# Performance work log

Measured on AMD Instinct MI355X. Metric: run time of the kernel, lower is better.

## Reference

```python
import jax, jax.numpy as jnp
import numpy as np

N = 50000      # nodes
IN = 128       # in_channels
H = 2          # heads
C = 64         # hidden_channels (per head)
E = 800000     # edges (before self-loops)
OUT = 40       # out_channels
BN_EPS = 1e-5
NEG_SLOPE = 0.2  # PyG GATConv default


def _bn(x, g, b):
    # BatchNorm1d forward with batch statistics (training-mode math, biased var)
    mu = jnp.mean(x, axis=0)
    v = jnp.var(x, axis=0)
    return (x - mu) * jax.lax.rsqrt(v + BN_EPS) * g + b


def _gat_conv(x, src, dst, W, a_src, a_dst, bias, concat):
    n = x.shape[0]
    h = (x @ W).reshape(n, H, C)                      # [N,H,C] per-head projection
    al_s = jnp.einsum('nhc,hc->nh', h, a_src)         # [N,H]
    al_d = jnp.einsum('nhc,hc->nh', h, a_dst)
    e = jax.nn.leaky_relu(al_s[src] + al_d[dst], NEG_SLOPE)  # [E,H]
    # segment softmax over edges sharing the same destination
    m = jax.ops.segment_max(e, dst, num_segments=n)
    ex = jnp.exp(e - m[dst])
    s = jax.ops.segment_sum(ex, dst, num_segments=n)
    alpha = ex / s[dst]                               # [E,H]
    out = jax.ops.segment_sum(h[src] * alpha[..., None], dst, num_segments=n)  # [N,H,C]
    out = out.reshape(n, H * C) if concat else out.mean(axis=1)
    return out + bias


def setup_inputs() -> dict:
    key = jax.random.key(0)
    ks = jax.random.split(key, 16)
    g = lambda k, shp, scale=1.0: jax.random.normal(k, shp, dtype=jnp.float32) * scale
    x = g(ks[0], (N, IN))
    edge_index = jax.random.randint(ks[1], (2, E), 0, N, dtype=jnp.int32)
    s = 1.0 / np.sqrt(IN)
    s2 = 1.0 / np.sqrt(H * C)
    return {
        'x': x,
        'edge_index': edge_index,
        'bn0_g': jnp.ones((IN,), jnp.float32), 'bn0_b': jnp.zeros((IN,), jnp.float32),
        'W1': g(ks[2], (IN, H * C), s), 'a1_src': g(ks[3], (H, C), s), 'a1_dst': g(ks[4], (H, C), s),
        'b1': jnp.zeros((H * C,), jnp.float32),
        'bn1_g': jnp.ones((H * C,), jnp.float32), 'bn1_b': jnp.zeros((H * C,), jnp.float32),
        'W2': g(ks[5], (H * C, H * C), s2), 'a2_src': g(ks[6], (H, C), s2), 'a2_dst': g(ks[7], (H, C), s2),
        'b2': jnp.zeros((C,), jnp.float32),
        'bn2_g': jnp.ones((C,), jnp.float32), 'bn2_b': jnp.zeros((C,), jnp.float32),
        'Wf': g(ks[8], (C, OUT), 1.0 / np.sqrt(C)), 'bf': jnp.zeros((OUT,), jnp.float32),
    }


def reference(x, edge_index, bn0_g, bn0_b, W1, a1_src, a1_dst, b1, bn1_g, bn1_b,
              W2, a2_src, a2_dst, b2, bn2_g, bn2_b, Wf, bf):
    n = x.shape[0]
    loop = jnp.arange(n, dtype=edge_index.dtype)
    src = jnp.concatenate([edge_index[0], loop])  # add self-loops (PyG default)
    dst = jnp.concatenate([edge_index[1], loop])
    h = _bn(x, bn0_g, bn0_b)
    # layer 1: concat heads
    h = _gat_conv(h, src, dst, W1, a1_src, a1_dst, b1, concat=True)
    h = jax.nn.elu(_bn(h, bn1_g, bn1_b))
    # (dropout is identity in eval mode)
    # layer 2: average heads
    h = _gat_conv(h, src, dst, W2, a2_src, a2_dst, b2, concat=False)
    h = jax.nn.elu(_bn(h, bn2_g, bn2_b))
    return h @ Wf + bf
```

## Files before the change

kernel.cpp:

```cpp
#include <hip/hip_runtime.h>
#include <hip/hip_fp16.h>


#define NEG_SLOPE 0.2f
#define BN_EPS 1e-5f
#define SH 15
#define NRANGE 16

typedef short bf16x8 __attribute__((ext_vector_type(8)));
typedef float f32x4 __attribute__((ext_vector_type(4)));

static __device__ __forceinline__ unsigned short f2bf(float f) {
    union { float f; unsigned u; } v; v.f = f;
    unsigned r = v.u + 0x7FFF + ((v.u >> 16) & 1);
    return (unsigned short)(r >> 16);
}
static __device__ __forceinline__ float2 bf2x2(unsigned v) {
    union { unsigned u; float f; } a, b;
    a.u = v << 16; b.u = v & 0xffff0000u;
    return make_float2(a.f, b.f);
}
static __device__ __forceinline__ float halfsel(unsigned p, int head) {
    __half2 h = *(__half2*)&p;
    return head ? __high2float(h) : __low2float(h);
}

template <int C>
static __device__ __forceinline__ void d_bnstat(const float* __restrict__ x, int M,
                                                int rowsPerBlock, float* __restrict__ sums,
                                                int b, float* red) {
    constexpr int TPR = C / 4;
    constexpr int RS  = 256 / TPR;
    const int t = threadIdx.x;
    const int cg = t % TPR, rg = t / TPR, w = t >> 6, lane = t & 63;
    int r0 = b * rowsPerBlock + rg;
    int r1 = min(M, b * rowsPerBlock + rowsPerBlock);
    float4 s = make_float4(0, 0, 0, 0), q = make_float4(0, 0, 0, 0);
    #pragma unroll 4
    for (int r = r0; r < r1; r += RS) {
        float4 v = *(const float4*)&x[(size_t)r * C + cg * 4];
        s.x += v.x; s.y += v.y; s.z += v.z; s.w += v.w;
        q.x += v.x * v.x; q.y += v.y * v.y; q.z += v.z * v.z; q.w += v.w * v.w;
    }
    #pragma unroll
    for (int off = TPR; off < 64; off <<= 1) {
        s.x += __shfl_xor(s.x, off); s.y += __shfl_xor(s.y, off);
        s.z += __shfl_xor(s.z, off); s.w += __shfl_xor(s.w, off);
        q.x += __shfl_xor(q.x, off); q.y += __shfl_xor(q.y, off);
        q.z += __shfl_xor(q.z, off); q.w += __shfl_xor(q.w, off);
    }
    if (lane < TPR) {
        *(float4*)&red[w * 2 * C + cg * 4] = s;
        *(float4*)&red[w * 2 * C + C + cg * 4] = q;
    }
    __syncthreads();
    for (int idx = t; idx < 2 * C; idx += 256) {
        float tot = red[idx] + red[2 * C + idx] + red[4 * C + idx] + red[6 * C + idx];
        atomicAdd(&sums[idx], tot);
    }
}

template <int C>
__global__ __launch_bounds__(256) void k_bnstat2(const float* __restrict__ x, int M,
                                                 int rowsPerBlock, float* __restrict__ sums) {
    __shared__ __align__(16) float red[4 * 2 * C];
    d_bnstat<C>(x, M, rowsPerBlock, sums, blockIdx.x, red);
}

__global__ __launch_bounds__(256) void k_prep(
    const int* __restrict__ ei, int E, int S, int NR,
    const float* __restrict__ x, int M, int bgrid,
    const float* __restrict__ W1, const float* __restrict__ W2,
    unsigned short* __restrict__ cnt, unsigned short* __restrict__ rank,
    float* __restrict__ sums,
    unsigned short* __restrict__ wt1, unsigned short* __restrict__ wt2) {
    __shared__ __align__(16) unsigned smem[3200];
    int b = blockIdx.x;
    int CG = NRANGE * S;
    if (b < CG) {
        unsigned* lcnt = smem;
        const int t = threadIdx.x;
        const int r = b & (NRANGE - 1), s = b >> 4;
        const unsigned lo = (unsigned)(r * NR);
        const int NRW = NR >> 1;
        for (int j = t; j < NRW; j += 256) lcnt[j] = 0;
        __syncthreads();
        int i1 = min(E, (s + 1) << SH);
        #pragma unroll 4
        for (int i = (s << SH) + t; i < i1; i += 256) {
            unsigned d = (unsigned)ei[E + i];
            unsigned rel = d - lo;
            if (rel < (unsigned)NR) {
                unsigned sh = (rel & 1) << 4;
                unsigned old = atomicAdd(&lcnt[rel >> 1], 1u << sh);
                rank[i] = (unsigned short)((old >> sh) & 0xffffu);
            }
        }
        __syncthreads();
        for (int j = t; j < NRW; j += 256) {
            int node = (int)lo + 2 * j;
            if (node < M)
                *(unsigned*)&cnt[(size_t)s * M + node] = lcnt[j];
        }
    } else if (b < CG + bgrid) {
        d_bnstat<128>(x, M, 256, sums, b - CG, (float*)smem);
    } else {
        int idx = (b - CG - bgrid) * 256 + threadIdx.x;
        if (idx < 128 * 128) {
            int n = idx >> 7, k = idx & 127;
            wt1[idx] = f2bf(W1[k * 128 + n]);
            wt2[idx] = f2bf(W2[k * 128 + n]);
        }
    }
}

__global__ __launch_bounds__(256) void k_scan(unsigned short* __restrict__ cnt,
                                              int Nn, int S,
                                              int* __restrict__ gcur,
                                              int* __restrict__ rowptr,
                                              unsigned short* __restrict__ degs) {
    __shared__ int wsum[4];
    __shared__ int s_base;
    int t = threadIdx.x, lane = t & 63, w = t >> 6;
    int i = blockIdx.x * 256 + t;
    int v = 0;
    if (i < Nn) {
        int run = 0;
        for (int s = 0; s < S; s++) {
            int cv = (int)cnt[(size_t)s * Nn + i];
            cnt[(size_t)s * Nn + i] = (unsigned short)run;
            run += cv;
        }
        v = run + 1;
    }
    int x = v;
    #pragma unroll
    for (int off = 1; off < 64; off <<= 1) {
        int y = __shfl_up(x, off);
        if (lane >= off) x += y;
    }
    if (lane == 63) wsum[w] = x;
    __syncthreads();
    if (t < 4) {
        int val = wsum[t];
        int xs = val;
        #pragma unroll
        for (int off = 1; off < 4; off <<= 1) {
            int y = __shfl_up(xs, off);
            if (t >= off) xs += y;
        }
        if (t == 3) s_base = atomicAdd(gcur, xs);
        wsum[t] = xs - val;
    }
    __syncthreads();
    if (i < Nn) {
        rowptr[i] = s_base + wsum[w] + (x - v);
        degs[i] = (unsigned short)v;
    }
}

static __device__ __forceinline__ void d_fill(int b, const int* __restrict__ ei,
                                              const unsigned short* __restrict__ rank,
                                              const unsigned short* __restrict__ pofs,
                                              const int* __restrict__ rowptr, int E, int Nn,
                                              unsigned short* __restrict__ ssrc) {
    int i = b * 256 + threadIdx.x;
    if (i < E) {
        int s = ei[i], d = ei[E + i];
        int p = i >> SH;
        int rk = (int)pofs[(size_t)p * Nn + d] + (int)rank[i];
        ssrc[rowptr[d] + 1 + rk] = (unsigned short)s;
    } else if (i < E + Nn) {
        int d = i - E;
        ssrc[rowptr[d]] = (unsigned short)d;
    }
}

static __device__ __forceinline__ void d_mfma(
    int blk, const float* __restrict__ A, const unsigned short* __restrict__ wt,
    const float* __restrict__ sums, const float* __restrict__ bng, const float* __restrict__ bnb,
    int elu, const float* __restrict__ asrc, const float* __restrict__ adst, int M,
    unsigned short* __restrict__ hb, float* __restrict__ als, float* __restrict__ ald) {
    __shared__ unsigned short As[64 * 136];
    __shared__ __align__(16) float stl[256];
    const int t = threadIdx.x;
    const int w = t >> 6, lane = t & 63;
    const int c = lane & 15, q = lane >> 4;
    const int row0 = blk * 64;

    if (t < 128) {
        float mu = sums[t] / (float)M;
        float var = sums[128 + t] / (float)M - mu * mu;
        float s = bng[t] * rsqrtf(var + BN_EPS);
        stl[t] = s;
        stl[128 + t] = bnb[t] - mu * s;
    }
    __syncthreads();

    const int gr = row0 + w * 16 + c;
    const bool rok = gr < M;

    float4 av[4][2];
    #pragma unroll
    for (int ks = 0; ks < 4; ks++) {
        const int cc = (ks * 4 + q) * 8;
        #pragma unroll
        for (int h = 0; h < 2; h++)
            av[ks][h] = rok ? *(const float4*)&A[(size_t)gr * 128 + cc + h * 4]
                            : make_float4(0.f, 0.f, 0.f, 0.f);
    }

    bf16x8 af[4];
    #pragma unroll
    for (int ks = 0; ks < 4; ks++) {
        const int cc = (ks * 4 + q) * 8;
        union { bf16x8 v; unsigned u[4]; } pk;
        #pragma unroll
        for (int h = 0; h < 2; h++) {
            float4 v = av[ks][h];
            if (rok) {
                float4 sc = *(const float4*)&stl[cc + h * 4];
                float4 sh = *(const float4*)&stl[128 + cc + h * 4];
                v.x = v.x * sc.x + sh.x; v.y = v.y * sc.y + sh.y;
                v.z = v.z * sc.z + sh.z; v.w = v.w * sc.w + sh.w;
                if (elu) {
                    v.x = v.x > 0.f ? v.x : expm1f(v.x);
                    v.y = v.y > 0.f ? v.y : expm1f(v.y);
                    v.z = v.z > 0.f ? v.z : expm1f(v.z);
                    v.w = v.w > 0.f ? v.w : expm1f(v.w);
                }
            }
            pk.u[h * 2]     = ((unsigned)f2bf(v.y) << 16) | f2bf(v.x);
            pk.u[h * 2 + 1] = ((unsigned)f2bf(v.w) << 16) | f2bf(v.z);
        }
        af[ks] = pk.v;
    }

    f32x4 acc[8] = {};
    #pragma unroll
    for (int half = 0; half < 2; half++) {
        bf16x8 br[8][2];
        #pragma unroll
        for (int tl = 0; tl < 8; tl++) {
            #pragma unroll
            for (int kk = 0; kk < 2; kk++)
                br[tl][kk] = *(const bf16x8*)&wt[(size_t)(tl * 16 + c) * 128 + ((half * 2 + kk) * 4 + q) * 8];
        }
        #pragma unroll
        for (int kk = 0; kk < 2; kk++) {
            #pragma unroll
            for (int tl = 0; tl < 8; tl++)
                acc[tl] = __builtin_amdgcn_mfma_f32_16x16x32_bf16(af[half * 2 + kk], br[tl][kk], acc[tl], 0, 0, 0);
        }
    }

    float as_[8], ad_[8];
    #pragma unroll
    for (int tl = 0; tl < 8; tl++) { as_[tl] = asrc[tl * 16 + c]; ad_[tl] = adst[tl * 16 + c]; }
    #pragma unroll
    for (int reg = 0; reg < 4; reg++) {
        float s0 = 0.f, s1 = 0.f, d0 = 0.f, d1 = 0.f;
        #pragma unroll
        for (int tl = 0; tl < 4; tl++) { s0 += acc[tl][reg] * as_[tl]; d0 += acc[tl][reg] * ad_[tl]; }
        #pragma unroll
        for (int tl = 4; tl < 8; tl++) { s1 += acc[tl][reg] * as_[tl]; d1 += acc[tl][reg] * ad_[tl]; }
        #pragma unroll
        for (int off = 1; off < 16; off <<= 1) {
            s0 += __shfl_xor(s0, off); s1 += __shfl_xor(s1, off);
            d0 += __shfl_xor(d0, off); d1 += __shfl_xor(d1, off);
        }
        int grow = row0 + w * 16 + q * 4 + reg;
        if (c == 0 && grow < M) {
            *(float2*)&als[(size_t)grow * 2] = make_float2(s0, s1);
            *(float2*)&ald[(size_t)grow * 2] = make_float2(d0, d1);
        }
    }

    #pragma unroll
    for (int reg = 0; reg < 4; reg++) {
        #pragma unroll
        for (int tl = 0; tl < 8; tl++)
            As[(w * 16 + q * 4 + reg) * 136 + tl * 16 + c] = f2bf(acc[tl][reg]);
    }
    #pragma unroll
    for (int j = 0; j < 4; j++) {
        int f = j * 64 + lane;
        int r = f >> 4, ch = f & 15;
        int grow = row0 + w * 16 + r;
        if (grow < M) {
            uint4 v = *(uint4*)&As[(w * 16 + r) * 136 + ch * 8];
            *(uint4*)&hb[(size_t)grow * 128 + ch * 8] = v;
        }
    }
}

__global__ __launch_bounds__(256) void k_mfma(
    const float* __restrict__ A, const unsigned short* __restrict__ wt,
    const float* __restrict__ sums, const float* __restrict__ bng, const float* __restrict__ bnb,
    int elu, const float* __restrict__ asrc, const float* __restrict__ adst, int M,
    unsigned short* __restrict__ hb, float* __restrict__ als, float* __restrict__ ald) {
    d_mfma(blockIdx.x, A, wt, sums, bng, bnb, elu, asrc, adst, M, hb, als, ald);
}

__global__ __launch_bounds__(256) void k_fill_mfma(
    const float* __restrict__ A, const unsigned short* __restrict__ wt,
    const float* __restrict__ sums, const float* __restrict__ bng, const float* __restrict__ bnb,
    const float* __restrict__ asrc, const float* __restrict__ adst, int M, int ggrid,
    unsigned short* __restrict__ hb, float* __restrict__ als, float* __restrict__ ald,
    const int* __restrict__ ei, const unsigned short* __restrict__ rank,
    const unsigned short* __restrict__ pofs,
    const int* __restrict__ rowptr, int E, int Nn, unsigned short* __restrict__ ssrc) {
    if (blockIdx.x < ggrid)
        d_mfma(blockIdx.x, A, wt, sums, bng, bnb, 0, asrc, adst, M, hb, als, ald);
    else
        d_fill(blockIdx.x - ggrid, ei, rank, pofs, rowptr, E, Nn, ssrc);
}

static __device__ __forceinline__ void acc8(float* acc, uint4 v, float a) {
    float2 p;
    p = bf2x2(v.x); acc[0] += a * p.x; acc[1] += a * p.y;
    p = bf2x2(v.y); acc[2] += a * p.x; acc[3] += a * p.y;
    p = bf2x2(v.z); acc[4] += a * p.x; acc[5] += a * p.y;
    p = bf2x2(v.w); acc[6] += a * p.x; acc[7] += a * p.y;
}

template <int MEAN>
static __device__ __forceinline__ void attnagg(
    const int* __restrict__ rowptr, const unsigned short* __restrict__ degs,
    const unsigned short* __restrict__ ssrc,
    const float* __restrict__ als, const float* __restrict__ ald,
    float* __restrict__ alpha, const unsigned short* __restrict__ hb,
    const float* __restrict__ bias, int Nn, float* __restrict__ out) {
    int gw = (blockIdx.x * blockDim.x + threadIdx.x) >> 6;
    if (gw >= Nn) return;
    int lane = threadIdx.x & 63;
    int sub = lane >> 4, c = lane & 15, head = c >> 3;
    int beg = rowptr[gw];
    int deg = (int)degs[gw];
    int end = beg + deg;
    float2 dv = *(const float2*)&ald[(size_t)gw * 2];
    float acc[8] = {};

    if (deg <= 64) {
        bool on = lane < deg;
        int eidx = beg + (on ? lane : 0);
        int sreg = (int)ssrc[eidx];
        float2 av = *(const float2*)&als[(size_t)sreg * 2];
        float v0 = av.x + dv.x; v0 = v0 > 0.f ? v0 : NEG_SLOPE * v0;
        float v1 = av.y + dv.y; v1 = v1 > 0.f ? v1 : NEG_SLOPE * v1;
        float p0 = on ? __expf(v0) : 0.f;
        float p1 = on ? __expf(v1) : 0.f;
        float t0 = p0, t1 = p1;
        #pragma unroll
        for (int off = 32; off; off >>= 1) {
            t0 += __shfl_xor(t0, off);
            t1 += __shfl_xor(t1, off);
        }
        __half2 hpk = __floats2half2_rn(p0 / t0, p1 / t1);
        unsigned pk = *(unsigned*)&hpk;

        int nit = (deg + 3) >> 2;
        int it = 0;
        for (; it + 4 <= nit; it += 4) {
            int s_[4]; float a_[4];
            #pragma unroll
            for (int u = 0; u < 4; u++) {
                int jj = (it + u) * 4 + sub;
                int ls = jj & 63;
                s_[u] = __shfl(sreg, ls);
                unsigned pw = (unsigned)__shfl(pk, ls);
                a_[u] = (jj < deg) ? halfsel(pw, head) : 0.f;
            }
            #pragma unroll
            for (int u = 0; u < 4; u++) {
                uint4 v = *(const uint4*)&hb[(size_t)s_[u] * 128 + c * 8];
                acc8(acc, v, a_[u]);
            }
        }
        for (; it < nit; it += 2) {
            const bool two = (it + 1) < nit;
            int s_[2]; float a_[2];
            #pragma unroll
            for (int u = 0; u < 2; u++) {
                if (u == 0 || two) {
                    int jj = (it + u) * 4 + sub;
                    int ls = jj & 63;
                    s_[u] = __shfl(sreg, ls);
                    unsigned pw = (unsigned)__shfl(pk, ls);
                    a_[u] = (jj < deg) ? halfsel(pw, head) : 0.f;
                }
            }
            #pragma unroll
            for (int u = 0; u < 2; u++) {
                if (u == 0 || two) {
                    uint4 v = *(const uint4*)&hb[(size_t)s_[u] * 128 + c * 8];
                    acc8(acc, v, a_[u]);
                }
            }
        }
    } else {
        float d0 = dv.x, d1 = dv.y;
        float m0 = -1e30f, m1 = -1e30f;
        for (int e = beg + lane; e < end; e += 64) {
            int s = (int)ssrc[e];
            float v0 = als[s * 2] + d0;     v0 = v0 > 0.f ? v0 : NEG_SLOPE * v0;
            float v1 = als[s * 2 + 1] + d1; v1 = v1 > 0.f ? v1 : NEG_SLOPE * v1;
            m0 = fmaxf(m0, v0); m1 = fmaxf(m1, v1);
        }
        #pragma unroll
        for (int off = 32; off; off >>= 1) {
            m0 = fmaxf(m0, __shfl_xor(m0, off));
            m1 = fmaxf(m1, __shfl_xor(m1, off));
        }
        float t0 = 0.f, t1 = 0.f;
        for (int e = beg + lane; e < end; e += 64) {
            int s = (int)ssrc[e];
            float v0 = als[s * 2] + d0;     v0 = v0 > 0.f ? v0 : NEG_SLOPE * v0;
            float v1 = als[s * 2 + 1] + d1; v1 = v1 > 0.f ? v1 : NEG_SLOPE * v1;
            float p0 = __expf(v0 - m0), p1 = __expf(v1 - m1);
            alpha[e * 2] = p0; alpha[e * 2 + 1] = p1;
            t0 += p0; t1 += p1;
        }
        #pragma unroll
        for (int off = 32; off; off >>= 1) {
            t0 += __shfl_xor(t0, off);
            t1 += __shfl_xor(t1, off);
        }
        float i0 = 1.f / t0, i1 = 1.f / t1;
        for (int e = beg + sub; e < end; e += 4) {
            int s = (int)ssrc[e];
            float a = (head ? alpha[(size_t)e * 2 + 1] * i1 : alpha[(size_t)e * 2] * i0);
            uint4 v = *(const uint4*)&hb[(size_t)s * 128 + c * 8];
            acc8(acc, v, a);
        }
    }

    #pragma unroll
    for (int j2 = 0; j2 < 8; j2++) {
        acc[j2] += __shfl_xor(acc[j2], 16);
        acc[j2] += __shfl_xor(acc[j2], 32);
        if (MEAN) acc[j2] += __shfl_xor(acc[j2], 8);
    }
    if (MEAN) {
        if (sub == 0 && c < 8) {
            float4 b0 = *(const float4*)&bias[c * 8];
            float4 b1 = *(const float4*)&bias[c * 8 + 4];
            float4 o0 = make_float4(0.5f * acc[0] + b0.x, 0.5f * acc[1] + b0.y, 0.5f * acc[2] + b0.z, 0.5f * acc[3] + b0.w);
            float4 o1 = make_float4(0.5f * acc[4] + b1.x, 0.5f * acc[5] + b1.y, 0.5f * acc[6] + b1.z, 0.5f * acc[7] + b1.w);
            *(float4*)&out[(size_t)gw * 64 + c * 8] = o0;
            *(float4*)&out[(size_t)gw * 64 + c * 8 + 4] = o1;
        }
    } else {
        if (sub == 0) {
            float4 b0 = *(const float4*)&bias[c * 8];
            float4 b1 = *(const float4*)&bias[c * 8 + 4];
            float4 o0 = make_float4(acc[0] + b0.x, acc[1] + b0.y, acc[2] + b0.z, acc[3] + b0.w);
            float4 o1 = make_float4(acc[4] + b1.x, acc[5] + b1.y, acc[6] + b1.z, acc[7] + b1.w);
            *(float4*)&out[(size_t)gw * 128 + c * 8] = o0;
            *(float4*)&out[(size_t)gw * 128 + c * 8 + 4] = o1;
        }
    }
}

__global__ __launch_bounds__(256) void k_attnagg1(const int* __restrict__ rowptr, const unsigned short* __restrict__ degs,
                                                  const unsigned short* __restrict__ ssrc,
                                                  const float* __restrict__ als, const float* __restrict__ ald,
                                                  float* __restrict__ alpha, const unsigned short* __restrict__ hb,
                                                  const float* __restrict__ bias, int Nn, float* __restrict__ out) {
    attnagg<0>(rowptr, degs, ssrc, als, ald, alpha, hb, bias, Nn, out);
}

__global__ __launch_bounds__(256) void k_attnagg2(const int* __restrict__ rowptr, const unsigned short* __restrict__ degs,
                                                  const unsigned short* __restrict__ ssrc,
                                                  const float* __restrict__ als, const float* __restrict__ ald,
                                                  float* __restrict__ alpha, const unsigned short* __restrict__ hb,
                                                  const float* __restrict__ bias, int Nn, float* __restrict__ out) {
    attnagg<1>(rowptr, degs, ssrc, als, ald, alpha, hb, bias, Nn, out);
}

__global__ __launch_bounds__(128) void k_gemmf(const float* __restrict__ A, const float* __restrict__ Wf,
                                               const float* __restrict__ bf,
                                               const float* __restrict__ sums, const float* __restrict__ bng,
                                               const float* __restrict__ bnb,
                                               int M, float* __restrict__ out) {
    __shared__ float As[128 * 65];
    __shared__ float Bs[64 * 40];
    __shared__ float stl[128];
    int t = threadIdx.x;
    int row0 = blockIdx.x * 128;
    if (t < 64) {
        float mu = sums[t] / (float)M;
        float var = sums[64 + t] / (float)M - mu * mu;
        float s = bng[t] * rsqrtf(var + BN_EPS);
        stl[t] = s;
        stl[64 + t] = bnb[t] - mu * s;
    }
    __syncthreads();
    for (int i = t; i < 64 * 40; i += 128) Bs[i] = Wf[i];
    for (int i = t; i < 128 * 64; i += 128) {
        int r = i >> 6, k = i & 63;
        int gr = row0 + r;
        float v = 0.f;
        if (gr < M) {
            v = A[(size_t)gr * 64 + k] * stl[k] + stl[64 + k];
            v = v > 0.f ? v : expm1f(v);
        }
        As[r * 65 + k] = v;
    }
    __syncthreads();
    int cg = t & 3, rg = t >> 2;
    float acc[4][10] = {};
    for (int k = 0; k < 64; k++) {
        float b[10];
        #pragma unroll
        for (int j = 0; j < 10; j++) b[j] = Bs[k * 40 + cg * 10 + j];
        #pragma unroll
        for (int r = 0; r < 4; r++) {
            float a = As[(rg * 4 + r) * 65 + k];
            #pragma unroll
            for (int j = 0; j < 10; j++) acc[r][j] += a * b[j];
        }
    }
    for (int r = 0; r < 4; r++) {
        int gr = row0 + rg * 4 + r;
        if (gr < M) {
            #pragma unroll
            for (int j = 0; j < 10; j++) out[(size_t)gr * 40 + cg * 10 + j] = acc[r][j] + bf[cg * 10 + j];
        }
    }
}

extern "C" void kernel_launch(void* const* d_in, const int* in_sizes, int n_in,
                              void* d_out, int out_size, void* d_ws, size_t ws_size,
                              hipStream_t stream) {
    const float* x     = (const float*)d_in[0];
    const int*   ei    = (const int*)d_in[1];
    const float* bn0_g = (const float*)d_in[2];
    const float* bn0_b = (const float*)d_in[3];
    const float* W1    = (const float*)d_in[4];
    const float* a1s   = (const float*)d_in[5];
    const float* a1d   = (const float*)d_in[6];
    const float* b1    = (const float*)d_in[7];
    const float* bn1_g = (const float*)d_in[8];
    const float* bn1_b = (const float*)d_in[9];
    const float* W2    = (const float*)d_in[10];
    const float* a2s   = (const float*)d_in[11];
    const float* a2d   = (const float*)d_in[12];
    const float* b2    = (const float*)d_in[13];
    const float* bn2_g = (const float*)d_in[14];
    const float* bn2_b = (const float*)d_in[15];
    const float* Wf    = (const float*)d_in[16];
    const float* bf    = (const float*)d_in[17];
    float* out = (float*)d_out;

    const int N  = in_sizes[0] / 128;
    const int E  = in_sizes[1] / 2;
    const int ET = E + N;
    const int S  = (E + (1 << SH) - 1) >> SH;
    const int NR = (((N + NRANGE - 1) / NRANGE) + 1) & ~1;

    char* ws = (char*)d_ws;
    size_t off = 0;
    auto alloc = [&](size_t bytes) -> char* {
        char* p = ws + off;
        off = (off + bytes + 255) & ~(size_t)255;
        return p;
    };
    float* sums   = (float*)alloc(644 * 4);
    int*   gcur   = (int*)(sums + 640);
    const size_t zlen = off;
    unsigned short* cnt = (unsigned short*)alloc((size_t)S * N * 2);
    int*   rowptr = (int*)alloc((size_t)N * 4);
    unsigned short* degs = (unsigned short*)alloc((size_t)N * 2);
    unsigned short* ssrc = (unsigned short*)alloc((size_t)ET * 2);
    unsigned short* rank = (unsigned short*)alloc((size_t)E * 2);
    float* abuf   = (float*)alloc((size_t)N * 128 * 4);
    unsigned short* hb  = (unsigned short*)alloc((size_t)N * 128 * 2);
    unsigned short* wt1 = (unsigned short*)alloc((size_t)128 * 128 * 2);
    unsigned short* wt2 = (unsigned short*)alloc((size_t)128 * 128 * 2);
    float* alpha  = (float*)alloc((size_t)ET * 2 * 4);
    float* als    = (float*)alloc((size_t)N * 2 * 4);
    float* ald    = (float*)alloc((size_t)N * 2 * 4);

    const int tb = 256;
    const int CG = NRANGE * S;
    const int bgrid = (N + 255) / 256;
    const int fgrid = (ET + tb - 1) / tb;
    const int wgrid = ((size_t)N * 64 + tb - 1) / tb;
    const int ggrid = (N + 63) / 64;

    hipMemsetAsync(ws, 0, zlen, stream);

    k_prep<<<CG + bgrid + 64, tb, 0, stream>>>(ei, E, S, NR, x, N, bgrid, W1, W2,
                                               cnt, rank, sums, wt1, wt2);
    k_scan<<<bgrid, tb, 0, stream>>>(cnt, N, S, gcur, rowptr, degs);

    k_fill_mfma<<<ggrid + fgrid, tb, 0, stream>>>(x, wt1, sums, bn0_g, bn0_b,
                                                  a1s, a1d, N, ggrid, hb, als, ald,
                                                  ei, rank, cnt, rowptr, E, N, ssrc);
    k_attnagg1<<<wgrid, tb, 0, stream>>>(rowptr, degs, ssrc, als, ald, alpha, hb, b1, N, abuf);

    k_bnstat2<128><<<bgrid, 256, 0, stream>>>(abuf, N, 256, sums + 256);

    k_mfma<<<ggrid, tb, 0, stream>>>(abuf, wt2, sums + 256, bn1_g, bn1_b, 1, a2s, a2d, N, hb, als, ald);
    k_attnagg2<<<wgrid, tb, 0, stream>>>(rowptr, degs, ssrc, als, ald, alpha, hb, b2, N, abuf);

    k_bnstat2<64><<<bgrid, 256, 0, stream>>>(abuf, N, 256, sums + 512);

    k_gemmf<<<(N + 127) / 128, 128, 0, stream>>>(abuf, Wf, bf, sums + 512, bn2_g, bn2_b, N, out);
}
```

Measured before the change: 349.4 us.

## Replace partitioned LDS counting sort with global atomic per-node counters

Edge-to-destination counting moves from a blocked scheme (edge chunks by node ranges, LDS 16-bit packed counters, per-chunk offsets scanned in k_scan) to one global int atomicAdd per edge that returns the rank directly. This removes the 16x re-reads of the destination array, the per-chunk count matrix and its serial per-node scan, and simplifies the fill step. In exchange it relies on global atomics contending on about 50k counters, and the order within each row becomes nondeterministic.

Result: faster. 332.6 us (-4.8%).

```diff
diff --git a/kernel.cpp b/kernel.cpp
--- a/kernel.cpp
+++ b/kernel.cpp
@@ -4,8 +4,6 @@
 
 #define NEG_SLOPE 0.2f
 #define BN_EPS 1e-5f
-#define SH 15
-#define NRANGE 16
 
 typedef short bf16x8 __attribute__((ext_vector_type(8)));
 typedef float f32x4 __attribute__((ext_vector_type(4)));
@@ -68,44 +66,24 @@
 }
 
 __global__ __launch_bounds__(256) void k_prep(
-    const int* __restrict__ ei, int E, int S, int NR,
+    const int* __restrict__ ei, int E, int rgrid,
     const float* __restrict__ x, int M, int bgrid,
     const float* __restrict__ W1, const float* __restrict__ W2,
-    unsigned short* __restrict__ cnt, unsigned short* __restrict__ rank,
+    int* __restrict__ cnt, unsigned short* __restrict__ rank,
     float* __restrict__ sums,
     unsigned short* __restrict__ wt1, unsigned short* __restrict__ wt2) {
-    __shared__ __align__(16) unsigned smem[3200];
+    __shared__ __align__(16) float red[4 * 2 * 128];
     int b = blockIdx.x;
-    int CG = NRANGE * S;
-    if (b < CG) {
-        unsigned* lcnt = smem;
-        const int t = threadIdx.x;
-        const int r = b & (NRANGE - 1), s = b >> 4;
-        const unsigned lo = (unsigned)(r * NR);
-        const int NRW = NR >> 1;
-        for (int j = t; j < NRW; j += 256) lcnt[j] = 0;
-        __syncthreads();
-        int i1 = min(E, (s + 1) << SH);
-        #pragma unroll 4
-        for (int i = (s << SH) + t; i < i1; i += 256) {
-            unsigned d = (unsigned)ei[E + i];
-            unsigned rel = d - lo;
-            if (rel < (unsigned)NR) {
-                unsigned sh = (rel & 1) << 4;
-                unsigned old = atomicAdd(&lcnt[rel >> 1], 1u << sh);
-                rank[i] = (unsigned short)((old >> sh) & 0xffffu);
-            }
-        }
-        __syncthreads();
-        for (int j = t; j < NRW; j += 256) {
-            int node = (int)lo + 2 * j;
-            if (node < M)
-                *(unsigned*)&cnt[(size_t)s * M + node] = lcnt[j];
-        }
-    } else if (b < CG + bgrid) {
-        d_bnstat<128>(x, M, 256, sums, b - CG, (float*)smem);
+    if (b < rgrid) {
+        int i = b * 256 + threadIdx.x;
+        if (i < E) {
+            int d = ei[E + i];
+            rank[i] = (unsigned short)atomicAdd(&cnt[d], 1);
+        }
+    } else if (b < rgrid + bgrid) {
+        d_bnstat<128>(x, M, 256, sums, b - rgrid, red);
     } else {
-        int idx = (b - CG - bgrid) * 256 + threadIdx.x;
+        int idx = (b - rgrid - bgrid) * 256 + threadIdx.x;
         if (idx < 128 * 128) {
             int n = idx >> 7, k = idx & 127;
             wt1[idx] = f2bf(W1[k * 128 + n]);
@@ -114,8 +92,7 @@
     }
 }
 
-__global__ __launch_bounds__(256) void k_scan(unsigned short* __restrict__ cnt,
-                                              int Nn, int S,
+__global__ __launch_bounds__(256) void k_scan(const int* __restrict__ cnt, int Nn,
                                               int* __restrict__ gcur,
                                               int* __restrict__ rowptr,
                                               unsigned short* __restrict__ degs) {
@@ -123,16 +100,7 @@
     __shared__ int s_base;
     int t = threadIdx.x, lane = t & 63, w = t >> 6;
     int i = blockIdx.x * 256 + t;
-    int v = 0;
-    if (i < Nn) {
-        int run = 0;
-        for (int s = 0; s < S; s++) {
-            int cv = (int)cnt[(size_t)s * Nn + i];
-            cnt[(size_t)s * Nn + i] = (unsigned short)run;
-            run += cv;
-        }
-        v = run + 1;
-    }
+    int v = (i < Nn) ? cnt[i] + 1 : 0;
     int x = v;
     #pragma unroll
     for (int off = 1; off < 64; off <<= 1) {
@@ -161,15 +129,12 @@
 
 static __device__ __forceinline__ void d_fill(int b, const int* __restrict__ ei,
                                               const unsigned short* __restrict__ rank,
-                                              const unsigned short* __restrict__ pofs,
                                               const int* __restrict__ rowptr, int E, int Nn,
                                               unsigned short* __restrict__ ssrc) {
     int i = b * 256 + threadIdx.x;
     if (i < E) {
         int s = ei[i], d = ei[E + i];
-        int p = i >> SH;
-        int rk = (int)pofs[(size_t)p * Nn + d] + (int)rank[i];
-        ssrc[rowptr[d] + 1 + rk] = (unsigned short)s;
+        ssrc[rowptr[d] + 1 + (int)rank[i]] = (unsigned short)s;
     } else if (i < E + Nn) {
         int d = i - E;
         ssrc[rowptr[d]] = (unsigned short)d;
@@ -308,12 +273,11 @@
     const float* __restrict__ asrc, const float* __restrict__ adst, int M, int ggrid,
     unsigned short* __restrict__ hb, float* __restrict__ als, float* __restrict__ ald,
     const int* __restrict__ ei, const unsigned short* __restrict__ rank,
-    const unsigned short* __restrict__ pofs,
     const int* __restrict__ rowptr, int E, int Nn, unsigned short* __restrict__ ssrc) {
     if (blockIdx.x < ggrid)
         d_mfma(blockIdx.x, A, wt, sums, bng, bnb, 0, asrc, adst, M, hb, als, ald);
     else
-        d_fill(blockIdx.x - ggrid, ei, rank, pofs, rowptr, E, Nn, ssrc);
+        d_fill(blockIdx.x - ggrid, ei, rank, rowptr, E, Nn, ssrc);
 }
 
 static __device__ __forceinline__ void acc8(float* acc, uint4 v, float a) {
@@ -556,8 +520,6 @@
     const int N  = in_sizes[0] / 128;
     const int E  = in_sizes[1] / 2;
     const int ET = E + N;
-    const int S  = (E + (1 << SH) - 1) >> SH;
-    const int NR = (((N + NRANGE - 1) / NRANGE) + 1) & ~1;
 
     char* ws = (char*)d_ws;
     size_t off = 0;
@@ -568,8 +530,8 @@
     };
     float* sums   = (float*)alloc(644 * 4);
     int*   gcur   = (int*)(sums + 640);
+    int*   cnt    = (int*)alloc((size_t)N * 4);
     const size_t zlen = off;
-    unsigned short* cnt = (unsigned short*)alloc((size_t)S * N * 2);
     int*   rowptr = (int*)alloc((size_t)N * 4);
     unsigned short* degs = (unsigned short*)alloc((size_t)N * 2);
     unsigned short* ssrc = (unsigned short*)alloc((size_t)ET * 2);
@@ -583,7 +545,7 @@
     float* ald    = (float*)alloc((size_t)N * 2 * 4);
 
     const int tb = 256;
-    const int CG = NRANGE * S;
+    const int rgrid = (E + tb - 1) / tb;
     const int bgrid = (N + 255) / 256;
     const int fgrid = (ET + tb - 1) / tb;
     const int wgrid = ((size_t)N * 64 + tb - 1) / tb;
@@ -591,13 +553,13 @@
 
     hipMemsetAsync(ws, 0, zlen, stream);
 
-    k_prep<<<CG + bgrid + 64, tb, 0, stream>>>(ei, E, S, NR, x, N, bgrid, W1, W2,
-                                               cnt, rank, sums, wt1, wt2);
-    k_scan<<<bgrid, tb, 0, stream>>>(cnt, N, S, gcur, rowptr, degs);
+    k_prep<<<rgrid + bgrid + 64, tb, 0, stream>>>(ei, E, rgrid, x, N, bgrid, W1, W2,
+                                                  cnt, rank, sums, wt1, wt2);
+    k_scan<<<bgrid, tb, 0, stream>>>(cnt, N, gcur, rowptr, degs);
 
     k_fill_mfma<<<ggrid + fgrid, tb, 0, stream>>>(x, wt1, sums, bn0_g, bn0_b,
                                                   a1s, a1d, N, ggrid, hb, als, ald,
-                                                  ei, rank, cnt, rowptr, E, N, ssrc);
+                                                  ei, rank, rowptr, E, N, ssrc);
     k_attnagg1<<<wgrid, tb, 0, stream>>>(rowptr, degs, ssrc, als, ald, alpha, hb, b1, N, abuf);
 
     k_bnstat2<128><<<bgrid, 256, 0, stream>>>(abuf, N, 256, sums + 256);
```
